# Kernel optimization log

Measured on AMD Instinct MI355X. Metric: run time of the kernel, lower is better.

Reference implementation:

```python
import jax, jax.numpy as jnp
import numpy as np

B, C_IN, C_OUT, N = 8, 256, 128, 4096
BN_EPS = 1e-5


def _conv1x1(w, b, t):
    # w: [out, in], t: [B, in, N] -> [B, out, N]
    return jnp.einsum('oc,bcn->bon', w, t) + b[None, :, None]


def setup_inputs() -> dict:
    key = jax.random.key(0)
    ks = jax.random.split(key, 11)
    s_in = 1.0 / np.sqrt(C_IN)
    s_out = 1.0 / np.sqrt(C_OUT)
    return {
        'x': jax.random.normal(ks[0], (B, C_IN, N), dtype=jnp.float32),
        'g_w': jax.random.normal(ks[1], (C_OUT, C_IN), dtype=jnp.float32) * s_in,
        'g_b': jax.random.normal(ks[2], (C_OUT,), dtype=jnp.float32) * s_in,
        'theta_w': jax.random.normal(ks[3], (C_OUT, C_IN), dtype=jnp.float32) * s_in,
        'theta_b': jax.random.normal(ks[4], (C_OUT,), dtype=jnp.float32) * s_in,
        'phi_w': jax.random.normal(ks[5], (C_OUT, C_IN), dtype=jnp.float32) * s_in,
        'phi_b': jax.random.normal(ks[6], (C_OUT,), dtype=jnp.float32) * s_in,
        'W_w': jax.random.normal(ks[7], (C_IN, C_OUT), dtype=jnp.float32) * s_out,
        'W_b': jax.random.normal(ks[8], (C_IN,), dtype=jnp.float32) * s_out,
        'bn_gamma': jax.random.uniform(ks[9], (C_IN,), dtype=jnp.float32),
        'bn_beta': jax.random.normal(ks[10], (C_IN,), dtype=jnp.float32) * 0.1,
    }


def reference(x, g_w, g_b, theta_w, theta_b, phi_w, phi_b, W_w, W_b, bn_gamma, bn_beta):
    n = x.shape[-1]
    g_x = _conv1x1(g_w, g_b, x)          # [B, Co, N]
    theta_x = _conv1x1(theta_w, theta_b, x)  # [B, Co, N]
    phi_x = _conv1x1(phi_w, phi_b, x)        # [B, Co, N]
    # f = theta_x^T @ phi_x, divided by N (no softmax) -> [B, N, N]
    f_div_c = jnp.einsum('bcn,bcm->bnm', theta_x, phi_x) / n
    # y[b,c,n] = sum_m f[b,n,m] * g_x[b,c,m]  -> already permuted to [B, Co, N]
    y = jnp.einsum('bnm,bcm->bcn', f_div_c, g_x)
    w_y = jnp.einsum('oc,bcn->bon', W_w, y) + W_b[None, :, None]  # [B, C_in, N]
    # BatchNorm1d, training mode: stats over (batch, spatial), biased variance
    mean = w_y.mean(axis=(0, 2), keepdims=True)
    var = w_y.var(axis=(0, 2), keepdims=True)
    w_y = (w_y - mean) * jax.lax.rsqrt(var + BN_EPS)
    w_y = w_y * bn_gamma[None, :, None] + bn_beta[None, :, None]
    return w_y + x  # generate=True residual
```

## Files before the change

kernel.cpp:

```cpp
#include <hip/hip_runtime.h>
#include <hip/hip_bf16.h>
#include <stdint.h>

#define BB   8
#define CIN  256
#define COUT 128
#define NN   4096

using f32x4  = __attribute__((ext_vector_type(4))) float;
using bf16x8 = __attribute__((ext_vector_type(8))) __bf16;
using u16x8  = __attribute__((ext_vector_type(8))) unsigned short;

static __device__ __forceinline__ unsigned short f2bf(float f) {
    unsigned int u = __builtin_bit_cast(unsigned int, f);
    u += 0x7FFFu + ((u >> 16) & 1u);
    return (unsigned short)(u >> 16);
}
static __device__ __forceinline__ float bf2f(unsigned short u) {
    return __builtin_bit_cast(float, (unsigned int)u << 16);
}
static __device__ __forceinline__ ushort4 pack4(float a, float b, float c, float d) {
    ushort4 r; r.x=f2bf(a); r.y=f2bf(b); r.z=f2bf(c); r.w=f2bf(d); return r;
}
#define MFMA(a,b,c) __builtin_amdgcn_mfma_f32_16x16x32_bf16((a),(b),(c),0,0,0)

static __device__ __forceinline__ int sw256(int r, int c) { return (r*256 + c) ^ ((r&7)<<3); }
static __device__ __forceinline__ int sw128(int r, int c) { return (r*128 + c) ^ ((r&7)<<3); }

__global__ __launch_bounds__(512) void kA(
    const float* __restrict__ x,
    unsigned short* __restrict__ Sp, float* __restrict__ Rp)
{
    __shared__ __align__(16) unsigned short SH[65536];
    int bid = blockIdx.x;
    int b = bid >> 4, ch = bid & 15;
    int n0 = ch * 256;
    int t = threadIdx.x, lane = t & 63, wv = t >> 6;
    int lr = lane & 15, lg = lane >> 4;

    const float* xb = x + (size_t)b*CIN*NN + n0;
    #pragma unroll
    for (int i = 0; i < 32; ++i) {
        int c = wv*32 + i;
        float4 f = *(const float4*)(xb + (size_t)c*NN + lane*4);
        float s = f.x + f.y + f.z + f.w;
        #pragma unroll
        for (int off = 1; off < 64; off <<= 1) s += __shfl_xor(s, off);
        if (lane == 0) Rp[bid*256 + c] = s;
        *(ushort4*)&SH[sw256(c, lane*4)] = pack4(f.x, f.y, f.z, f.w);
    }
    __syncthreads();

    int wr = wv >> 1, wc = wv & 1;
    f32x4 acc[4][8];
    #pragma unroll
    for (int i = 0; i < 4; ++i)
        #pragma unroll
        for (int j = 0; j < 8; ++j) acc[i][j] = (f32x4){0.f,0.f,0.f,0.f};
    #pragma unroll
    for (int ks = 0; ks < 8; ++ks) {
        bf16x8 af[4], bfr[8];
        #pragma unroll
        for (int mi = 0; mi < 4; ++mi) {
            int row = wr*64 + mi*16 + lr;
            af[mi] = __builtin_bit_cast(bf16x8, *(const u16x8*)&SH[sw256(row, ks*32 + lg*8)]);
        }
        #pragma unroll
        for (int ni = 0; ni < 8; ++ni) {
            int row = wc*128 + ni*16 + lr;
            bfr[ni] = __builtin_bit_cast(bf16x8, *(const u16x8*)&SH[sw256(row, ks*32 + lg*8)]);
        }
        #pragma unroll
        for (int mi = 0; mi < 4; ++mi)
            #pragma unroll
            for (int ni = 0; ni < 8; ++ni)
                acc[mi][ni] = MFMA(af[mi], bfr[ni], acc[mi][ni]);
    }
    unsigned short* dst = Sp + (size_t)bid * 65536;
    #pragma unroll
    for (int mi = 0; mi < 4; ++mi)
        #pragma unroll
        for (int ni = 0; ni < 8; ++ni)
            #pragma unroll
            for (int j = 0; j < 4; ++j) {
                int c1 = wr*64 + mi*16 + lg*4 + j;
                int c2 = wc*128 + ni*16 + lr;
                dst[c1*256 + c2] = f2bf(acc[mi][ni][j]);
            }
}

__global__ __launch_bounds__(512) void kRP(
    const unsigned short* __restrict__ Sp, const float* __restrict__ Rp,
    const float* __restrict__ Wwf, const float* __restrict__ gwf,
    const float* __restrict__ twf, const float* __restrict__ pwf,
    const float* __restrict__ gbv, const float* __restrict__ pbv, const float* __restrict__ tbv,
    unsigned short* __restrict__ Sbf, float* __restrict__ rv,
    unsigned short* __restrict__ Abf, unsigned short* __restrict__ CmT,
    float* __restrict__ a1, float* __restrict__ c1v, float* __restrict__ p2,
    float* __restrict__ params, float* __restrict__ stats)
{
    __shared__ __align__(16) unsigned short Ls[32768];
    __shared__ __align__(16) unsigned short Rs[32768];
    int bid = blockIdx.x;
    int t = threadIdx.x, lane = t & 63, wv = t >> 6;
    int lr = lane & 15, lg = lane >> 4;

    if (bid < 128) {
        int b = bid >> 4, sl = bid & 15;
        int base = sl*4096 + t*8;
        float s[8] = {0.f,0.f,0.f,0.f,0.f,0.f,0.f,0.f};
        #pragma unroll
        for (int i = 0; i < 16; ++i) {
            u16x8 v = *(const u16x8*)(Sp + (size_t)(b*16 + i)*65536 + base);
            #pragma unroll
            for (int e = 0; e < 8; ++e) s[e] += bf2f(v[e]);
        }
        u16x8 o;
        #pragma unroll
        for (int e = 0; e < 8; ++e) o[e] = f2bf(s[e]);
        *(u16x8*)(Sbf + (size_t)b*65536 + base) = o;
        return;
    }
    if (bid < 136) {
        int b = bid - 128;
        if (t < 256) {
            float s = 0.f;
            #pragma unroll
            for (int i = 0; i < 16; ++i) s += Rp[(b*16 + i)*256 + t];
            rv[b*256 + t] = s;
        }
        return;
    }

    if (bid == 136) {
        for (int i = t; i < 8192; i += 512) {
            int flat = i*4, r = flat >> 7, c = flat & 127;
            float4 f = *(const float4*)(Wwf + flat);
            *(ushort4*)&Ls[sw128(r, c)] = pack4(f.x, f.y, f.z, f.w);
        }
        {
            int c = lane * 4;  int k4 = wv * 4;
            #pragma unroll
            for (int rep = 0; rep < 4; ++rep) {
                int kb = rep*32 + k4;
                float4 f0 = *(const float4*)(gwf + (size_t)(kb+0)*256 + c);
                float4 f1 = *(const float4*)(gwf + (size_t)(kb+1)*256 + c);
                float4 f2 = *(const float4*)(gwf + (size_t)(kb+2)*256 + c);
                float4 f3 = *(const float4*)(gwf + (size_t)(kb+3)*256 + c);
                *(ushort4*)&Rs[sw128(c+0, kb)] = pack4(f0.x, f1.x, f2.x, f3.x);
                *(ushort4*)&Rs[sw128(c+1, kb)] = pack4(f0.y, f1.y, f2.y, f3.y);
                *(ushort4*)&Rs[sw128(c+2, kb)] = pack4(f0.z, f1.z, f2.z, f3.z);
                *(ushort4*)&Rs[sw128(c+3, kb)] = pack4(f0.w, f1.w, f2.w, f3.w);
            }
        }
        if (t < 512) stats[t] = 0.f;
    } else {
        {
            int c = lane * 4;  int k4 = wv * 4;
            #pragma unroll
            for (int rep = 0; rep < 4; ++rep) {
                int kb = rep*32 + k4;
                float4 f0 = *(const float4*)(twf + (size_t)(kb+0)*256 + c);
                float4 f1 = *(const float4*)(twf + (size_t)(kb+1)*256 + c);
                float4 f2 = *(const float4*)(twf + (size_t)(kb+2)*256 + c);
                float4 f3 = *(const float4*)(twf + (size_t)(kb+3)*256 + c);
                *(ushort4*)&Ls[sw128(c+0, kb)] = pack4(f0.x, f1.x, f2.x, f3.x);
                *(ushort4*)&Ls[sw128(c+1, kb)] = pack4(f0.y, f1.y, f2.y, f3.y);
                *(ushort4*)&Ls[sw128(c+2, kb)] = pack4(f0.z, f1.z, f2.z, f3.z);
                *(ushort4*)&Ls[sw128(c+3, kb)] = pack4(f0.w, f1.w, f2.w, f3.w);
                float4 g0 = *(const float4*)(pwf + (size_t)(kb+0)*256 + c);
                float4 g1 = *(const float4*)(pwf + (size_t)(kb+1)*256 + c);
                float4 g2 = *(const float4*)(pwf + (size_t)(kb+2)*256 + c);
                float4 g3 = *(const float4*)(pwf + (size_t)(kb+3)*256 + c);
                *(ushort4*)&Rs[sw128(c+0, kb)] = pack4(g0.x, g1.x, g2.x, g3.x);
                *(ushort4*)&Rs[sw128(c+1, kb)] = pack4(g0.y, g1.y, g2.y, g3.y);
                *(ushort4*)&Rs[sw128(c+2, kb)] = pack4(g0.z, g1.z, g2.z, g3.z);
                *(ushort4*)&Rs[sw128(c+3, kb)] = pack4(g0.w, g1.w, g2.w, g3.w);
            }
        }
    }
    __syncthreads();

    int wr = wv >> 2, wc = wv & 3;
    f32x4 acc[8][4];
    #pragma unroll
    for (int i = 0; i < 8; ++i)
        #pragma unroll
        for (int j = 0; j < 4; ++j) acc[i][j] = (f32x4){0.f,0.f,0.f,0.f};
    #pragma unroll
    for (int ks = 0; ks < 4; ++ks) {
        bf16x8 af[8], bfr[4];
        #pragma unroll
        for (int mi = 0; mi < 8; ++mi) {
            int r = wr*128 + mi*16 + lr;
            af[mi] = __builtin_bit_cast(bf16x8, *(const u16x8*)&Ls[sw128(r, ks*32 + lg*8)]);
        }
        #pragma unroll
        for (int ni = 0; ni < 4; ++ni) {
            int c = wc*64 + ni*16 + lr;
            bfr[ni] = __builtin_bit_cast(bf16x8, *(const u16x8*)&Rs[sw128(c, ks*32 + lg*8)]);
        }
        #pragma unroll
        for (int mi = 0; mi < 8; ++mi)
            #pragma unroll
            for (int ni = 0; ni < 4; ++ni)
                acc[mi][ni] = MFMA(af[mi], bfr[ni], acc[mi][ni]);
    }
    unsigned short* Dst = (bid == 136) ? Abf : CmT;
    #pragma unroll
    for (int mi = 0; mi < 8; ++mi)
        #pragma unroll
        for (int ni = 0; ni < 4; ++ni)
            #pragma unroll
            for (int j = 0; j < 4; ++j) {
                int r = wr*128 + mi*16 + lg*4 + j;
                int c = wc*64 + ni*16 + lr;
                Dst[r*256 + c] = f2bf(acc[mi][ni][j]);
            }

    if (bid == 136) {
        if (t < 256) {
            float s = 0.f;
            #pragma unroll
            for (int q = 0; q < 32; ++q) {
                float4 f = *(const float4*)(Wwf + (size_t)t*128 + q*4);
                s += f.x*gbv[q*4] + f.y*gbv[q*4+1] + f.z*gbv[q*4+2] + f.w*gbv[q*4+3];
            }
            a1[t] = s;
        }
    } else {
        if (t < 256) {
            float s1 = 0.f, s2 = 0.f;
            for (int k = 0; k < 128; ++k) {
                s1 += twf[(size_t)k*256 + t] * pbv[k];
                s2 += pwf[(size_t)k*256 + t] * tbv[k];
            }
            c1v[t] = s1; p2[t] = s2;
        }
        if (t < 64) {
            float v = pbv[t]*tbv[t] + pbv[t+64]*tbv[t+64];
            #pragma unroll
            for (int off = 1; off < 64; off <<= 1) v += __shfl_xor(v, off);
            if (t == 0) params[0] = v;
        }
    }
}

__global__ __launch_bounds__(512) void kE(
    const unsigned short* __restrict__ Sbf, const float* __restrict__ rv,
    const unsigned short* __restrict__ Abf, const unsigned short* __restrict__ CmT,
    const float* __restrict__ a1g, const float* __restrict__ c1vg, const float* __restrict__ p2g,
    const float* __restrict__ params, const float* __restrict__ Wbv,
    unsigned short* __restrict__ Ebf, float* __restrict__ fv, float* __restrict__ stats)
{
    __shared__ __align__(16) unsigned short Ybuf[16384];
    __shared__ __align__(16) unsigned short Ebuf[16384];
    __shared__ float r_l[256], p2_l[256], c1v_l[256], cr[256];
    __shared__ float a1_l[64], ar[64], Yp2[64], er[64], diag_l[64];
    __shared__ float rp2_s;
    int blk = blockIdx.x;
    int b = blk >> 2, obase = (blk & 3) * 64;
    int t = threadIdx.x, lane = t & 63, wv = t >> 6;
    int lr = lane & 15, lg = lane >> 4;
    const float invN = 1.0f/4096.0f;
    const unsigned short* Sb = Sbf + (size_t)b*65536;

    if (t < 256) {
        r_l[t] = rv[b*256 + t];
        p2_l[t] = p2g[t];
        c1v_l[t] = c1vg[t];
    } else if (t < 320) {
        a1_l[t - 256] = a1g[obase + (t - 256)];
    }
    __syncthreads();

    f32x4 acc[4][2];
    #pragma unroll
    for (int i = 0; i < 4; ++i) { acc[i][0] = (f32x4){0,0,0,0}; acc[i][1] = (f32x4){0,0,0,0}; }
    const unsigned short* Arow0 = Abf + (size_t)obase*256;
    #pragma unroll
    for (int ks = 0; ks < 8; ++ks) {
        bf16x8 a4[4], b2[2];
        #pragma unroll
        for (int mi = 0; mi < 4; ++mi)
            a4[mi] = __builtin_bit_cast(bf16x8, *(const u16x8*)(Arow0 + (size_t)(mi*16+lr)*256 + ks*32 + lg*8));
        #pragma unroll
        for (int ni = 0; ni < 2; ++ni)
            b2[ni] = __builtin_bit_cast(bf16x8, *(const u16x8*)(Sb + (size_t)(wv*32+ni*16+lr)*256 + ks*32 + lg*8));
        #pragma unroll
        for (int mi = 0; mi < 4; ++mi)
            #pragma unroll
            for (int ni = 0; ni < 2; ++ni)
                acc[mi][ni] = MFMA(a4[mi], b2[ni], acc[mi][ni]);
    }
    #pragma unroll
    for (int mi = 0; mi < 4; ++mi)
        #pragma unroll
        for (int ni = 0; ni < 2; ++ni)
            #pragma unroll
            for (int j = 0; j < 4; ++j) {
                int ol = mi*16 + lg*4 + j;
                int c2 = wv*32 + ni*16 + lr;
                Ybuf[ol*256 + (c2 ^ ((ol&7)<<3))] = f2bf(acc[mi][ni][j]);
            }
    __syncthreads();

    {
        int row = t >> 3, p8 = t & 7;
        float sA = 0.f, sY = 0.f;
        const unsigned short* Ar = Abf + (size_t)(obase + row)*256 + p8*32;
        #pragma unroll
        for (int q = 0; q < 4; ++q) {
            u16x8 av = *(const u16x8*)(Ar + q*8);
            #pragma unroll
            for (int e = 0; e < 8; ++e) {
                int c = p8*32 + q*8 + e;
                sA += bf2f(av[e]) * r_l[c];
                sY += bf2f(Ybuf[row*256 + (c ^ ((row&7)<<3))]) * p2_l[c];
            }
        }
        sA += __shfl_xor(sA, 1); sA += __shfl_xor(sA, 2); sA += __shfl_xor(sA, 4);
        sY += __shfl_xor(sY, 1); sY += __shfl_xor(sY, 2); sY += __shfl_xor(sY, 4);
        if (p8 == 0) { ar[row] = sA; Yp2[row] = sY; }
    }
    if (t < 256) {
        float s = 0.f;
        const unsigned short* Cr = CmT + (size_t)t*256;
        #pragma unroll
        for (int q = 0; q < 32; ++q) {
            u16x8 v = *(const u16x8*)(Cr + q*8);
            #pragma unroll
            for (int e = 0; e < 8; ++e) s += bf2f(v[e]) * r_l[q*8 + e];
        }
        cr[t] = s;
    }
    if (t < 64) {
        float v = r_l[t*4]*p2_l[t*4] + r_l[t*4+1]*p2_l[t*4+1]
                + r_l[t*4+2]*p2_l[t*4+2] + r_l[t*4+3]*p2_l[t*4+3];
        #pragma unroll
        for (int off = 1; off < 64; off <<= 1) v += __shfl_xor(v, off);
        if (t == 0) rp2_s = v;
    }
    __syncthreads();

    f32x4 accE[4][2];
    #pragma unroll
    for (int i = 0; i < 4; ++i) { accE[i][0] = (f32x4){0,0,0,0}; accE[i][1] = (f32x4){0,0,0,0}; }
    #pragma unroll
    for (int ks = 0; ks < 8; ++ks) {
        bf16x8 a4[4], b2[2];
        #pragma unroll
        for (int mi = 0; mi < 4; ++mi) {
            int ol = mi*16 + lr;
            a4[mi] = __builtin_bit_cast(bf16x8, *(const u16x8*)&Ybuf[ol*256 + ((ks*32 + lg*8) ^ ((ol&7)<<3))]);
        }
        #pragma unroll
        for (int ni = 0; ni < 2; ++ni)
            b2[ni] = __builtin_bit_cast(bf16x8, *(const u16x8*)(CmT + (size_t)(wv*32+ni*16+lr)*256 + ks*32 + lg*8));
        #pragma unroll
        for (int mi = 0; mi < 4; ++mi)
            #pragma unroll
            for (int ni = 0; ni < 2; ++ni)
                accE[mi][ni] = MFMA(a4[mi], b2[ni], accE[mi][ni]);
    }
    unsigned short* Eb = Ebf + (size_t)b*65536;
    #pragma unroll
    for (int mi = 0; mi < 4; ++mi)
        #pragma unroll
        for (int ni = 0; ni < 2; ++ni)
            #pragma unroll
            for (int j = 0; j < 4; ++j) {
                int ol = mi*16 + lg*4 + j;
                int cp = wv*32 + ni*16 + lr;
                float e = accE[mi][ni][j]*invN + a1_l[ol]*invN*cr[cp]
                        + (invN*ar[ol] + a1_l[ol])*c1v_l[cp];
                unsigned short eb = f2bf(e);
                Ebuf[ol*256 + (cp ^ ((ol&7)<<3))] = eb;
                Eb[(size_t)(obase + ol)*256 + cp] = eb;
            }
    __syncthreads();

    float f_reg = 0.f;
    {
        int row = t >> 3, p8 = t & 7;
        float s = 0.f;
        #pragma unroll
        for (int q = 0; q < 4; ++q)
            #pragma unroll
            for (int e = 0; e < 8; ++e) {
                int c = p8*32 + q*8 + e;
                s += bf2f(Ebuf[row*256 + (c ^ ((row&7)<<3))]) * r_l[c];
            }
        s += __shfl_xor(s, 1); s += __shfl_xor(s, 2); s += __shfl_xor(s, 4);
        if (p8 == 0) er[row] = s;
    }
    if (t < 64) {
        diag_l[t] = 0.f;
        float sg = params[0];
        f_reg = invN*(Yp2[t] + a1_l[t]*rp2_s + ar[t]*sg) + a1_l[t]*sg + Wbv[obase + t];
        fv[b*256 + obase + t] = f_reg;
    }
    __syncthreads();

    f32x4 accZ[4][2];
    #pragma unroll
    for (int i = 0; i < 4; ++i) { accZ[i][0] = (f32x4){0,0,0,0}; accZ[i][1] = (f32x4){0,0,0,0}; }
    #pragma unroll
    for (int ks = 0; ks < 8; ++ks) {
        bf16x8 a4[4], b2[2];
        #pragma unroll
        for (int mi = 0; mi < 4; ++mi) {
            int ol = mi*16 + lr;
            a4[mi] = __builtin_bit_cast(bf16x8, *(const u16x8*)&Ebuf[ol*256 + ((ks*32 + lg*8) ^ ((ol&7)<<3))]);
        }
        #pragma unroll
        for (int ni = 0; ni < 2; ++ni)
            b2[ni] = __builtin_bit_cast(bf16x8, *(const u16x8*)(Sb + (size_t)(wv*32+ni*16+lr)*256 + ks*32 + lg*8));
        #pragma unroll
        for (int mi = 0; mi < 4; ++mi)
            #pragma unroll
            for (int ni = 0; ni < 2; ++ni)
                accZ[mi][ni] = MFMA(a4[mi], b2[ni], accZ[mi][ni]);
    }
    #pragma unroll
    for (int mi = 0; mi < 4; ++mi)
        #pragma unroll
        for (int j = 0; j < 4; ++j) {
            int ol = mi*16 + lg*4 + j;
            float s = 0.f;
            #pragma unroll
            for (int ni = 0; ni < 2; ++ni) {
                int c2 = wv*32 + ni*16 + lr;
                s += accZ[mi][ni][j] * bf2f(Ebuf[ol*256 + (c2 ^ ((ol&7)<<3))]);
            }
            s += __shfl_xor(s, 1); s += __shfl_xor(s, 2);
            s += __shfl_xor(s, 4); s += __shfl_xor(s, 8);
            if (lr == 0) atomicAdd(&diag_l[ol], s);
        }
    __syncthreads();

    if (t < 64) {
        int o = obase + t;
        atomicAdd(&stats[o], er[t] + 4096.0f*f_reg);
        atomicAdd(&stats[256 + o], diag_l[t] + 2.0f*f_reg*er[t] + 4096.0f*f_reg*f_reg);
    }
}

__global__ __launch_bounds__(512) void kF(
    const float* __restrict__ x, const unsigned short* __restrict__ Ebf,
    const float* __restrict__ fv, const float* __restrict__ stats,
    const float* __restrict__ gamma, const float* __restrict__ beta,
    float* __restrict__ out)
{
    __shared__ __align__(16) unsigned short Xs[128*256];
    __shared__ float scale_l[256], shift_l[256];
    int b = blockIdx.x >> 5, n0 = (blockIdx.x & 31) * 128;
    int t = threadIdx.x, lane = t & 63, wv = t >> 6, lr = lane & 15, lg = lane >> 4;
    const float inv = 1.0f / 32768.0f;
    if (t < 256) {
        float mu  = stats[t] * inv;
        float var = stats[256 + t] * inv - mu*mu;
        float sc  = gamma[t] * rsqrtf(var + 1e-5f);
        scale_l[t] = sc;
        shift_l[t] = (fv[b*256 + t] - mu) * sc + beta[t];
    }
    {
        int nq = (t & 31) * 4, c0 = (t >> 5) * 4;
        const float* xb = x + (size_t)b*CIN*NN + n0 + nq;
        #pragma unroll
        for (int p = 0; p < 4; ++p) {
            int c = p*64 + c0;
            const float* xp = xb + (size_t)c*NN;
            float4 f0 = *(const float4*)(xp);
            float4 f1 = *(const float4*)(xp + NN);
            float4 f2 = *(const float4*)(xp + 2*NN);
            float4 f3 = *(const float4*)(xp + 3*NN);
            *(ushort4*)&Xs[(nq+0)*256 + (c ^ (((nq+0)&7)<<3))] = pack4(f0.x,f1.x,f2.x,f3.x);
            *(ushort4*)&Xs[(nq+1)*256 + (c ^ (((nq+1)&7)<<3))] = pack4(f0.y,f1.y,f2.y,f3.y);
            *(ushort4*)&Xs[(nq+2)*256 + (c ^ (((nq+2)&7)<<3))] = pack4(f0.z,f1.z,f2.z,f3.z);
            *(ushort4*)&Xs[(nq+3)*256 + (c ^ (((nq+3)&7)<<3))] = pack4(f0.w,f1.w,f2.w,f3.w);
        }
    }
    __syncthreads();

    int wn = wv >> 2, wo = wv & 3;
    int nb = wn*64, ob = wo*64;
    const unsigned short* Eb = Ebf + (size_t)b*65536;
    f32x4 acc[4][4];
    #pragma unroll
    for (int i = 0; i < 4; ++i)
        #pragma unroll
        for (int j = 0; j < 4; ++j) acc[i][j] = (f32x4){0,0,0,0};

    #pragma unroll
    for (int ks = 0; ks < 8; ++ks) {
        bf16x8 xf[4], ef[4];
        #pragma unroll
        for (int ni = 0; ni < 4; ++ni) {
            int n = nb + ni*16 + lr;
            xf[ni] = __builtin_bit_cast(bf16x8, *(const u16x8*)&Xs[(n*256 + ks*32 + lg*8) ^ ((n&7)<<3)]);
        }
        #pragma unroll
        for (int oi = 0; oi < 4; ++oi) {
            int o = ob + oi*16 + lr;
            ef[oi] = __builtin_bit_cast(bf16x8, *(const u16x8*)(Eb + (size_t)o*256 + ks*32 + lg*8));
        }
        #pragma unroll
        for (int ni = 0; ni < 4; ++ni)
            #pragma unroll
            for (int oi = 0; oi < 4; ++oi)
                acc[ni][oi] = MFMA(xf[ni], ef[oi], acc[ni][oi]);
    }

    float* op = out + (size_t)b*CIN*NN;
    #pragma unroll
    for (int oi = 0; oi < 4; ++oi) {
        int o = ob + oi*16 + lr;
        float sc = scale_l[o], sh = shift_l[o];
        #pragma unroll
        for (int ni = 0; ni < 4; ++ni) {
            int nbase = nb + ni*16 + lg*4;
            float4 st;
            float* sp_ = &st.x;
            #pragma unroll
            for (int j = 0; j < 4; ++j) {
                int n = nbase + j;
                sp_[j] = acc[ni][oi][j]*sc + sh + bf2f(Xs[(n*256 + o) ^ ((n&7)<<3)]);
            }
            *(float4*)(op + (size_t)o*NN + n0 + nbase) = st;
        }
    }
}

extern "C" void kernel_launch(void* const* d_in, const int* in_sizes, int n_in,
                              void* d_out, int out_size, void* d_ws, size_t ws_size,
                              hipStream_t stream)
{
    (void)in_sizes; (void)n_in; (void)out_size; (void)ws_size;
    const float* x     = (const float*)d_in[0];
    const float* gw    = (const float*)d_in[1];
    const float* gb    = (const float*)d_in[2];
    const float* tw    = (const float*)d_in[3];
    const float* tb    = (const float*)d_in[4];
    const float* pw    = (const float*)d_in[5];
    const float* pb    = (const float*)d_in[6];
    const float* Ww    = (const float*)d_in[7];
    const float* Wb    = (const float*)d_in[8];
    const float* gamma = (const float*)d_in[9];
    const float* beta  = (const float*)d_in[10];
    float* out = (float*)d_out;

    char* ws = (char*)d_ws;
    unsigned short* Sp  = (unsigned short*)(ws + 0);
    float* Rp           = (float*)(ws + 16777216);
    unsigned short* Sbf = (unsigned short*)(ws + 16908288);
    float* rv           = (float*)(ws + 17956864);
    unsigned short* Abf = (unsigned short*)(ws + 17965056);
    unsigned short* CmT = (unsigned short*)(ws + 18096128);
    unsigned short* Ebf = (unsigned short*)(ws + 18227200);
    float* fv           = (float*)(ws + 19275776);
    float* a1           = (float*)(ws + 19283968);
    float* c1v          = (float*)(ws + 19284992);
    float* p2           = (float*)(ws + 19286016);
    float* params       = (float*)(ws + 19287040);
    float* stats        = (float*)(ws + 19287104);

    kA <<<128, 512, 0, stream>>>(x, Sp, Rp);
    kRP<<<138, 512, 0, stream>>>(Sp, Rp, Ww, gw, tw, pw, gb, pb, tb,
                                 Sbf, rv, Abf, CmT, a1, c1v, p2, params, stats);
    kE <<<32,  512, 0, stream>>>(Sbf, rv, Abf, CmT, a1, c1v, p2, params, Wb, Ebf, fv, stats);
    kF <<<256, 512, 0, stream>>>(x, Ebf, fv, stats, gamma, beta, out);
}
```

Measured before the change: 100.8 us.

## Move weight-product blocks into Gram kernel, stage Gram stores through LDS, transpose final MFMA

The two weight-product blocks (Abf and CmT) now run alongside the per-chunk Gram computation in the first kernel instead of alongside the reduction. This shortens the critical path of the reduction kernel and shrinks it to a plain partial-sum pass. Gram tile results are staged through swizzled shared memory so global stores become 16-byte vectors instead of scattered 2-byte writes. The final kernel swaps MFMA operand order so each lane writes consecutive n along a row, though its stores become scalar rather than float4.

```diff
diff --git a/kernel.cpp b/kernel.cpp
--- a/kernel.cpp
+++ b/kernel.cpp
@@ -29,110 +29,84 @@
 
 __global__ __launch_bounds__(512) void kA(
     const float* __restrict__ x,
-    unsigned short* __restrict__ Sp, float* __restrict__ Rp)
-{
-    __shared__ __align__(16) unsigned short SH[65536];
-    int bid = blockIdx.x;
-    int b = bid >> 4, ch = bid & 15;
-    int n0 = ch * 256;
-    int t = threadIdx.x, lane = t & 63, wv = t >> 6;
-    int lr = lane & 15, lg = lane >> 4;
-
-    const float* xb = x + (size_t)b*CIN*NN + n0;
-    #pragma unroll
-    for (int i = 0; i < 32; ++i) {
-        int c = wv*32 + i;
-        float4 f = *(const float4*)(xb + (size_t)c*NN + lane*4);
-        float s = f.x + f.y + f.z + f.w;
-        #pragma unroll
-        for (int off = 1; off < 64; off <<= 1) s += __shfl_xor(s, off);
-        if (lane == 0) Rp[bid*256 + c] = s;
-        *(ushort4*)&SH[sw256(c, lane*4)] = pack4(f.x, f.y, f.z, f.w);
-    }
-    __syncthreads();
-
-    int wr = wv >> 1, wc = wv & 1;
-    f32x4 acc[4][8];
-    #pragma unroll
-    for (int i = 0; i < 4; ++i)
-        #pragma unroll
-        for (int j = 0; j < 8; ++j) acc[i][j] = (f32x4){0.f,0.f,0.f,0.f};
-    #pragma unroll
-    for (int ks = 0; ks < 8; ++ks) {
-        bf16x8 af[4], bfr[8];
-        #pragma unroll
-        for (int mi = 0; mi < 4; ++mi) {
-            int row = wr*64 + mi*16 + lr;
-            af[mi] = __builtin_bit_cast(bf16x8, *(const u16x8*)&SH[sw256(row, ks*32 + lg*8)]);
-        }
-        #pragma unroll
-        for (int ni = 0; ni < 8; ++ni) {
-            int row = wc*128 + ni*16 + lr;
-            bfr[ni] = __builtin_bit_cast(bf16x8, *(const u16x8*)&SH[sw256(row, ks*32 + lg*8)]);
-        }
-        #pragma unroll
-        for (int mi = 0; mi < 4; ++mi)
-            #pragma unroll
-            for (int ni = 0; ni < 8; ++ni)
-                acc[mi][ni] = MFMA(af[mi], bfr[ni], acc[mi][ni]);
-    }
-    unsigned short* dst = Sp + (size_t)bid * 65536;
-    #pragma unroll
-    for (int mi = 0; mi < 4; ++mi)
-        #pragma unroll
-        for (int ni = 0; ni < 8; ++ni)
-            #pragma unroll
-            for (int j = 0; j < 4; ++j) {
-                int c1 = wr*64 + mi*16 + lg*4 + j;
-                int c2 = wc*128 + ni*16 + lr;
-                dst[c1*256 + c2] = f2bf(acc[mi][ni][j]);
-            }
-}
-
-__global__ __launch_bounds__(512) void kRP(
-    const unsigned short* __restrict__ Sp, const float* __restrict__ Rp,
     const float* __restrict__ Wwf, const float* __restrict__ gwf,
     const float* __restrict__ twf, const float* __restrict__ pwf,
     const float* __restrict__ gbv, const float* __restrict__ pbv, const float* __restrict__ tbv,
-    unsigned short* __restrict__ Sbf, float* __restrict__ rv,
+    unsigned short* __restrict__ Sp, float* __restrict__ Rp,
     unsigned short* __restrict__ Abf, unsigned short* __restrict__ CmT,
     float* __restrict__ a1, float* __restrict__ c1v, float* __restrict__ p2,
     float* __restrict__ params, float* __restrict__ stats)
 {
-    __shared__ __align__(16) unsigned short Ls[32768];
-    __shared__ __align__(16) unsigned short Rs[32768];
+    __shared__ __align__(16) unsigned short SH[65536];
     int bid = blockIdx.x;
     int t = threadIdx.x, lane = t & 63, wv = t >> 6;
     int lr = lane & 15, lg = lane >> 4;
 
     if (bid < 128) {
-        int b = bid >> 4, sl = bid & 15;
-        int base = sl*4096 + t*8;
-        float s[8] = {0.f,0.f,0.f,0.f,0.f,0.f,0.f,0.f};
-        #pragma unroll
-        for (int i = 0; i < 16; ++i) {
-            u16x8 v = *(const u16x8*)(Sp + (size_t)(b*16 + i)*65536 + base);
-            #pragma unroll
-            for (int e = 0; e < 8; ++e) s[e] += bf2f(v[e]);
-        }
-        u16x8 o;
-        #pragma unroll
-        for (int e = 0; e < 8; ++e) o[e] = f2bf(s[e]);
-        *(u16x8*)(Sbf + (size_t)b*65536 + base) = o;
+        int b = bid >> 4, ch = bid & 15;
+        int n0 = ch * 256;
+        const float* xb = x + (size_t)b*CIN*NN + n0;
+        #pragma unroll
+        for (int i = 0; i < 32; ++i) {
+            int c = wv*32 + i;
+            float4 f = *(const float4*)(xb + (size_t)c*NN + lane*4);
+            float s = f.x + f.y + f.z + f.w;
+            #pragma unroll
+            for (int off = 1; off < 64; off <<= 1) s += __shfl_xor(s, off);
+            if (lane == 0) Rp[bid*256 + c] = s;
+            *(ushort4*)&SH[sw256(c, lane*4)] = pack4(f.x, f.y, f.z, f.w);
+        }
+        __syncthreads();
+
+        int wr = wv >> 1, wc = wv & 1;
+        f32x4 acc[4][8];
+        #pragma unroll
+        for (int i = 0; i < 4; ++i)
+            #pragma unroll
+            for (int j = 0; j < 8; ++j) acc[i][j] = (f32x4){0.f,0.f,0.f,0.f};
+        #pragma unroll
+        for (int ks = 0; ks < 8; ++ks) {
+            bf16x8 af[4], bfr[8];
+            #pragma unroll
+            for (int mi = 0; mi < 4; ++mi) {
+                int row = wr*64 + mi*16 + lr;
+                af[mi] = __builtin_bit_cast(bf16x8, *(const u16x8*)&SH[sw256(row, ks*32 + lg*8)]);
+            }
+            #pragma unroll
+            for (int ni = 0; ni < 8; ++ni) {
+                int row = wc*128 + ni*16 + lr;
+                bfr[ni] = __builtin_bit_cast(bf16x8, *(const u16x8*)&SH[sw256(row, ks*32 + lg*8)]);
+            }
+            #pragma unroll
+            for (int mi = 0; mi < 4; ++mi)
+                #pragma unroll
+                for (int ni = 0; ni < 8; ++ni)
+                    acc[mi][ni] = MFMA(af[mi], bfr[ni], acc[mi][ni]);
+        }
+        __syncthreads();
+        #pragma unroll
+        for (int mi = 0; mi < 4; ++mi)
+            #pragma unroll
+            for (int ni = 0; ni < 8; ++ni)
+                #pragma unroll
+                for (int j = 0; j < 4; ++j) {
+                    int c1 = wr*64 + mi*16 + lg*4 + j;
+                    int c2 = wc*128 + ni*16 + lr;
+                    SH[sw256(c1, c2)] = f2bf(acc[mi][ni][j]);
+                }
+        __syncthreads();
+        unsigned short* dst = Sp + (size_t)bid * 65536;
+        #pragma unroll
+        for (int i = t; i < 8192; i += 512) {
+            int row = i >> 5, q = i & 31;
+            *(u16x8*)(dst + row*256 + ((q ^ (row&7)) * 8)) = *(const u16x8*)&SH[row*256 + q*8];
+        }
         return;
     }
-    if (bid < 136) {
-        int b = bid - 128;
-        if (t < 256) {
-            float s = 0.f;
-            #pragma unroll
-            for (int i = 0; i < 16; ++i) s += Rp[(b*16 + i)*256 + t];
-            rv[b*256 + t] = s;
-        }
-        return;
-    }
-
-    if (bid == 136) {
+
+    unsigned short* Ls = SH;
+    unsigned short* Rs = SH + 32768;
+    if (bid == 128) {
         for (int i = t; i < 8192; i += 512) {
             int flat = i*4, r = flat >> 7, c = flat & 127;
             float4 f = *(const float4*)(Wwf + flat);
@@ -206,7 +180,7 @@
             for (int ni = 0; ni < 4; ++ni)
                 acc[mi][ni] = MFMA(af[mi], bfr[ni], acc[mi][ni]);
     }
-    unsigned short* Dst = (bid == 136) ? Abf : CmT;
+    unsigned short* Dst = (bid == 128) ? Abf : CmT;
     #pragma unroll
     for (int mi = 0; mi < 8; ++mi)
         #pragma unroll
@@ -218,7 +192,7 @@
                 Dst[r*256 + c] = f2bf(acc[mi][ni][j]);
             }
 
-    if (bid == 136) {
+    if (bid == 128) {
         if (t < 256) {
             float s = 0.f;
             #pragma unroll
@@ -242,6 +216,36 @@
             #pragma unroll
             for (int off = 1; off < 64; off <<= 1) v += __shfl_xor(v, off);
             if (t == 0) params[0] = v;
+        }
+    }
+}
+
+__global__ __launch_bounds__(512) void kR(
+    const unsigned short* __restrict__ Sp, const float* __restrict__ Rp,
+    unsigned short* __restrict__ Sbf, float* __restrict__ rv)
+{
+    int bid = blockIdx.x, t = threadIdx.x;
+    if (bid < 128) {
+        int b = bid >> 4, sl = bid & 15;
+        int base = sl*4096 + t*8;
+        float s[8] = {0.f,0.f,0.f,0.f,0.f,0.f,0.f,0.f};
+        #pragma unroll
+        for (int i = 0; i < 16; ++i) {
+            u16x8 v = *(const u16x8*)(Sp + (size_t)(b*16 + i)*65536 + base);
+            #pragma unroll
+            for (int e = 0; e < 8; ++e) s[e] += bf2f(v[e]);
+        }
+        u16x8 o;
+        #pragma unroll
+        for (int e = 0; e < 8; ++e) o[e] = f2bf(s[e]);
+        *(u16x8*)(Sbf + (size_t)b*65536 + base) = o;
+    } else {
+        int b = bid - 128;
+        if (t < 256) {
+            float s = 0.f;
+            #pragma unroll
+            for (int i = 0; i < 16; ++i) s += Rp[(b*16 + i)*256 + t];
+            rv[b*256 + t] = s;
         }
     }
 }
@@ -506,28 +510,25 @@
             ef[oi] = __builtin_bit_cast(bf16x8, *(const u16x8*)(Eb + (size_t)o*256 + ks*32 + lg*8));
         }
         #pragma unroll
-        for (int ni = 0; ni < 4; ++ni)
-            #pragma unroll
-            for (int oi = 0; oi < 4; ++oi)
-                acc[ni][oi] = MFMA(xf[ni], ef[oi], acc[ni][oi]);
-    }
-
-    float* op = out + (size_t)b*CIN*NN;
+        for (int oi = 0; oi < 4; ++oi)
+            #pragma unroll
+            for (int ni = 0; ni < 4; ++ni)
+                acc[oi][ni] = MFMA(ef[oi], xf[ni], acc[oi][ni]);
+    }
+
+    float* op = out + (size_t)b*CIN*NN + n0;
     #pragma unroll
     for (int oi = 0; oi < 4; ++oi) {
-        int o = ob + oi*16 + lr;
-        float sc = scale_l[o], sh = shift_l[o];
-        #pragma unroll
-        for (int ni = 0; ni < 4; ++ni) {
-            int nbase = nb + ni*16 + lg*4;
-            float4 st;
-            float* sp_ = &st.x;
-            #pragma unroll
-            for (int j = 0; j < 4; ++j) {
-                int n = nbase + j;
-                sp_[j] = acc[ni][oi][j]*sc + sh + bf2f(Xs[(n*256 + o) ^ ((n&7)<<3)]);
-            }
-            *(float4*)(op + (size_t)o*NN + n0 + nbase) = st;
+        #pragma unroll
+        for (int j = 0; j < 4; ++j) {
+            int o = ob + oi*16 + lg*4 + j;
+            float sc = scale_l[o], sh = shift_l[o];
+            #pragma unroll
+            for (int ni = 0; ni < 4; ++ni) {
+                int n = nb + ni*16 + lr;
+                float val = acc[oi][ni][j]*sc + sh + bf2f(Xs[(n*256 + (o ^ ((n&7)<<3)))]);
+                op[(size_t)o*NN + n] = val;
+            }
         }
     }
 }
@@ -565,9 +566,9 @@
     float* params       = (float*)(ws + 19287040);
     float* stats        = (float*)(ws + 19287104);
 
-    kA <<<128, 512, 0, stream>>>(x, Sp, Rp);
-    kRP<<<138, 512, 0, stream>>>(Sp, Rp, Ww, gw, tw, pw, gb, pb, tb,
-                                 Sbf, rv, Abf, CmT, a1, c1v, p2, params, stats);
-    kE <<<32,  512, 0, stream>>>(Sbf, rv, Abf, CmT, a1, c1v, p2, params, Wb, Ebf, fv, stats);
-    kF <<<256, 512, 0, stream>>>(x, Ebf, fv, stats, gamma, beta, out);
-}
+    kA<<<130, 512, 0, stream>>>(x, Ww, gw, tw, pw, gb, pb, tb,
+                                Sp, Rp, Abf, CmT, a1, c1v, p2, params, stats);
+    kR<<<136, 512, 0, stream>>>(Sp, Rp, Sbf, rv);
+    kE<<<32,  512, 0, stream>>>(Sbf, rv, Abf, CmT, a1, c1v, p2, params, Wb, Ebf, fv, stats);
+    kF<<<256, 512, 0, stream>>>(x, Ebf, fv, stats, gamma, beta, out);
+}
```

Result: faster. 90.04 us (-10.7%).
